# Kernel optimization log

Measured on AMD Instinct MI355X. Metric: run time of the kernel, lower is better.

The kernel has to match this reference:

```python
import jax, jax.numpy as jnp
import numpy as np

EPS = 1e-5

def _ste(x, q):
    # straight-through estimator: forward=q, backward=identity
    return x + jax.lax.stop_gradient(q - x)

def act_quant(x):
    # per-token int8 absmax quantization (BitNet b1.58 style), fake-quantized
    scale = 127.0 / jnp.clip(jnp.max(jnp.abs(x), axis=-1, keepdims=True), EPS)
    q = jnp.clip(jnp.round(x * scale), -128.0, 127.0) / scale
    return _ste(x, q)

def weight_quant(w):
    # ternary {-1,0,1} weights scaled by mean absolute value
    s = jnp.clip(jnp.mean(jnp.abs(w)), EPS)
    q = jnp.clip(jnp.round(w / s), -1.0, 1.0) * s
    return _ste(w, q)

def bit_linear(x, w):
    # x: [..., in], w: [out, in]
    return jnp.einsum('bsi,oi->bso', act_quant(x), weight_quant(w))

def setup_inputs() -> dict:
    key = jax.random.key(0)
    k1, k2, k3 = jax.random.split(key, 3)
    d_model, hidden = 2048, 4 * 2048
    x = jax.random.normal(k1, (4, 2048, d_model), dtype=jnp.float32)
    w1 = jax.random.normal(k2, (hidden, d_model), dtype=jnp.float32) * 0.02
    w2 = jax.random.normal(k3, (d_model, hidden), dtype=jnp.float32) * 0.02
    return {"x": x, "w1": w1, "w2": w2}

def reference(x, w1, w2):
    h = bit_linear(x, w1)            # [B, S, 4*d]
    h = jax.nn.gelu(h, approximate=False)  # exact erf GELU (nn.GELU default)
    return bit_linear(h, w2)         # [B, S, d]
```

## Files before the change

### kernel.cpp

```cpp
#include <hip/hip_runtime.h>
#include <hip/hip_bf16.h>
#include <hip/hip_fp16.h>
#include <stdint.h>

#define TPB 256
#define EPSF 1e-5f

using i32x4 = __attribute__((ext_vector_type(4))) int;


__device__ __forceinline__ void gload16(const void* g, void* l) {
    __builtin_amdgcn_global_load_lds(
        (__attribute__((address_space(1))) void*)g,
        (__attribute__((address_space(3))) void*)l,
        16, 0, 0);
}

__device__ __forceinline__ float wave_reduce_sum(float v) {
#pragma unroll
    for (int off = 32; off > 0; off >>= 1) v += __shfl_down(v, off, 64);
    return v;
}

__device__ __forceinline__ float wave_reduce_max(float v) {
#pragma unroll
    for (int off = 32; off > 0; off >>= 1) v = fmaxf(v, __shfl_down(v, off, 64));
    return v;
}

__device__ __forceinline__ int q8(float f, float scale, float lo, float hi) {
    return (int)fminf(fmaxf(rintf(f * scale), lo), hi);
}

__device__ __forceinline__ float gelu_fast(float x) {
    float x2 = x * x;
    float u = x * (0.7978845608f + 0.0356774081f * x2);
    float e = exp2f(u * -2.8853900817779268f);
    return x * __builtin_amdgcn_rcpf(1.0f + e);
}


__global__ void abssum_partial(const float* __restrict__ w, int n4,
                               float* __restrict__ part) {
    const float4* w4 = (const float4*)w;
    float acc = 0.f;
    for (int i = blockIdx.x * TPB + threadIdx.x; i < n4; i += gridDim.x * TPB) {
        float4 v = w4[i];
        acc += fabsf(v.x) + fabsf(v.y) + fabsf(v.z) + fabsf(v.w);
    }
    acc = wave_reduce_sum(acc);
    __shared__ float sh[4];
    if ((threadIdx.x & 63) == 0) sh[threadIdx.x >> 6] = acc;
    __syncthreads();
    if (threadIdx.x == 0) part[blockIdx.x] = sh[0] + sh[1] + sh[2] + sh[3];
}

__global__ void finalize_scales(const float* __restrict__ part1,
                                const float* __restrict__ part2,
                                float* __restrict__ scales, int nparts, float inv_n) {
    float a = 0.f, b = 0.f;
    for (int i = threadIdx.x; i < nparts; i += TPB) { a += part1[i]; b += part2[i]; }
    a = wave_reduce_sum(a);
    b = wave_reduce_sum(b);
    __shared__ float sa[4], sb[4];
    if ((threadIdx.x & 63) == 0) { sa[threadIdx.x >> 6] = a; sb[threadIdx.x >> 6] = b; }
    __syncthreads();
    if (threadIdx.x == 0) {
        scales[0] = fmaxf((sa[0] + sa[1] + sa[2] + sa[3]) * inv_n, EPSF);
        scales[1] = fmaxf((sb[0] + sb[1] + sb[2] + sb[3]) * inv_n, EPSF);
    }
}


__global__ void quant_w_i8(const float* __restrict__ w,
                           signed char* __restrict__ wq,
                           const float* __restrict__ scales, int sidx, int n4) {
    const float inv = 1.0f / scales[sidx];
    const float4* w4 = (const float4*)w;
    unsigned* oq = (unsigned*)wq;
    for (int i = blockIdx.x * TPB + threadIdx.x; i < n4; i += gridDim.x * TPB) {
        float4 v = w4[i];
        unsigned p = ((unsigned)(q8(v.x, inv, -1.f, 1.f) & 0xff)) |
                     ((unsigned)(q8(v.y, inv, -1.f, 1.f) & 0xff) << 8) |
                     ((unsigned)(q8(v.z, inv, -1.f, 1.f) & 0xff) << 16) |
                     ((unsigned)(q8(v.w, inv, -1.f, 1.f) & 0xff) << 24);
        oq[i] = p;
    }
}


template <int NF4>
__global__ void quant_x_i8(const float* __restrict__ in,
                           signed char* __restrict__ outq,
                           float* __restrict__ dq, int cols) {
    const long long row = blockIdx.x;
    const float4* r4 = (const float4*)(in + row * (long long)cols);
    float4 v[NF4];
    float mx = 0.f;
#pragma unroll
    for (int j = 0; j < NF4; ++j) {
        v[j] = r4[threadIdx.x + TPB * j];
        mx = fmaxf(mx, fmaxf(fmaxf(fabsf(v[j].x), fabsf(v[j].y)),
                             fmaxf(fabsf(v[j].z), fabsf(v[j].w))));
    }
    mx = wave_reduce_max(mx);
    __shared__ float sh[4];
    __shared__ float res;
    if ((threadIdx.x & 63) == 0) sh[threadIdx.x >> 6] = mx;
    __syncthreads();
    if (threadIdx.x == 0) res = fmaxf(fmaxf(sh[0], sh[1]), fmaxf(sh[2], sh[3]));
    __syncthreads();
    const float clipped = fmaxf(res, EPSF);
    const float scale = 127.f / clipped;
    if (threadIdx.x == 0) dq[row] = clipped / 127.f;
    unsigned* oq = (unsigned*)(outq + row * (long long)cols);
#pragma unroll
    for (int j = 0; j < NF4; ++j) {
        unsigned p = ((unsigned)(q8(v[j].x, scale, -128.f, 127.f) & 0xff)) |
                     ((unsigned)(q8(v[j].y, scale, -128.f, 127.f) & 0xff) << 8) |
                     ((unsigned)(q8(v[j].z, scale, -128.f, 127.f) & 0xff) << 16) |
                     ((unsigned)(q8(v[j].w, scale, -128.f, 127.f) & 0xff) << 24);
        oq[threadIdx.x + TPB * j] = p;
    }
}


template <int NJ>
__global__ void quant_h_i8(const unsigned short* __restrict__ h,
                           signed char* __restrict__ outq,
                           float* __restrict__ dq, int cols) {
    const long long row = blockIdx.x;
    const unsigned short* rp = h + row * (long long)cols;
    uint4 v[NJ];
    float mx = 0.f;
#pragma unroll
    for (int j = 0; j < NJ; ++j) {
        v[j] = *(const uint4*)(rp + (threadIdx.x + TPB * j) * 8);
        const unsigned* u = (const unsigned*)&v[j];
#pragma unroll
        for (int e = 0; e < 4; ++e) {
            float2 f2 = __half22float2(*(const __half2*)&u[e]);
            mx = fmaxf(mx, fmaxf(fabsf(f2.x), fabsf(f2.y)));
        }
    }
    mx = wave_reduce_max(mx);
    __shared__ float sh[4];
    __shared__ float res;
    if ((threadIdx.x & 63) == 0) sh[threadIdx.x >> 6] = mx;
    __syncthreads();
    if (threadIdx.x == 0) res = fmaxf(fmaxf(sh[0], sh[1]), fmaxf(sh[2], sh[3]));
    __syncthreads();
    const float clipped = fmaxf(res, EPSF);
    const float scale = 127.f / clipped;
    if (threadIdx.x == 0) dq[row] = clipped / 127.f;
    uint2* oq = (uint2*)(outq + row * (long long)cols);
#pragma unroll
    for (int j = 0; j < NJ; ++j) {
        const unsigned* u = (const unsigned*)&v[j];
        unsigned o[2] = {0, 0};
#pragma unroll
        for (int e = 0; e < 4; ++e) {
            float2 f2 = __half22float2(*(const __half2*)&u[e]);
            unsigned b0 = (unsigned)(q8(f2.x, scale, -128.f, 127.f) & 0xff);
            unsigned b1 = (unsigned)(q8(f2.y, scale, -128.f, 127.f) & 0xff);
            o[e >> 1] |= (b0 | (b1 << 8)) << ((e & 1) * 16);
        }
        oq[threadIdx.x + TPB * j] = *(uint2*)o;
    }
}


__device__ __forceinline__ void stage_half(const char* Xb, long long rowB, int prow,
                                           int tk, char* dst, int tid, int cbs) {
    const long long gc = (long long)tk * 128 + cbs;
    const int r = tid >> 3;
    gload16(Xb + (long long)(prow + r) * rowB + gc, dst + tid * 16);
    gload16(Xb + (long long)(prow + 64 + r) * rowB + gc, dst + 8192 + tid * 16);
}

#define QUAD(MB, NB)                                                            \
    _Pragma("unroll") for (int mi = 0; mi < 4; ++mi)                            \
    _Pragma("unroll") for (int ni = 0; ni < 2; ++ni)                            \
    _Pragma("unroll") for (int ks = 0; ks < 2; ++ks)                            \
        acc[(MB)*4 + mi][(NB)*2 + ni] = __builtin_amdgcn_mfma_i32_16x16x64_i8(  \
            aq[mi][ks], bq[(NB)*2 + ni][ks], acc[(MB)*4 + mi][(NB)*2 + ni], 0, 0, 0);


__global__ __launch_bounds__(512, 2) void gemm1p(
    const signed char* __restrict__ A, const signed char* __restrict__ B,
    unsigned short* __restrict__ C, int N, int K,
    const float* __restrict__ dq, const float* __restrict__ scales, int ntile) {
    __shared__ __align__(16) char lds[131072];

    const int tid = threadIdx.x;
    const int lane = tid & 63;
    const int wid = tid >> 6;
    const int wr = wid >> 2;
    const int wc = wid & 3;

    const unsigned gx = gridDim.x;
    unsigned lin = blockIdx.y * gx + blockIdx.x;
    const unsigned qq = (gx * gridDim.y) >> 3;
    lin = (lin & 7) * qq + (lin >> 3);
    const unsigned bx = lin % gx;
    const unsigned byg = lin / gx;

    const int n0 = (int)bx * 256;
    const long long rb = (long long)K;
    const char* Ab = (const char*)A;
    const char* Bb = (const char*)B;

    const int NTT = ntile << 4;

    const int cbs = (((tid & 7) ^ ((tid >> 3) & 7)) << 4);
    const int l15 = lane & 15, l4 = lane >> 4;
    const int swz = (lane & 7) << 4;
    const int acb0 = (l4 * 16) ^ swz;
    const int acb1 = (64 + l4 * 16) ^ swz;
    const int aoff = wr * 16384;
    const int boff = 32768 + (wc >> 1) * 16384 + (wc & 1) * 8192;

    i32x4 acc[8][4] = {};
    i32x4 aq[4][2], bq[4][2];

    auto mrow = [&](int v) -> int { return ((int)byg * ntile + (v >> 4)) * 256; };

    stage_half(Bb, rb, n0, 0, lds + 32768, tid, cbs);
    stage_half(Bb, rb, n0 + 128, 0, lds + 32768 + 16384, tid, cbs);
    stage_half(Ab, rb, mrow(0), 0, lds + 0, tid, cbs);
    stage_half(Ab, rb, mrow(0) + 128, 0, lds + 16384, tid, cbs);
    stage_half(Bb, rb, n0, 1, lds + 65536 + 32768, tid, cbs);
    stage_half(Bb, rb, n0 + 128, 1, lds + 65536 + 32768 + 16384, tid, cbs);
    stage_half(Ab, rb, mrow(1), 1, lds + 65536, tid, cbs);
    asm volatile("s_waitcnt vmcnt(6)" ::: "memory");
    __builtin_amdgcn_sched_barrier(0);
    __builtin_amdgcn_s_barrier();

    const float s = scales[0];

    for (int vt = 0; vt < NTT; ++vt) {
        char* cur = lds + ((vt & 1) << 16);
        char* nxt = lds + (((vt + 1) & 1) << 16);
        const bool s1 = (vt + 1) < NTT;
        const bool s2 = (vt + 2) < NTT;
        const int k1 = (vt + 1) & 15;
        const int k2 = (vt + 2) & 15;

#pragma unroll
        for (int mi = 0; mi < 4; ++mi) {
            const char* p = cur + aoff + (mi * 16 + l15) * 128;
            aq[mi][0] = *(const i32x4*)(p + acb0);
            aq[mi][1] = *(const i32x4*)(p + acb1);
        }
#pragma unroll
        for (int ni = 0; ni < 4; ++ni) {
            const char* p = cur + boff + (ni * 16 + l15) * 128;
            bq[ni][0] = *(const i32x4*)(p + acb0);
            bq[ni][1] = *(const i32x4*)(p + acb1);
        }
        if (s1) stage_half(Ab, rb, mrow(vt + 1) + 128, k1, nxt + 16384, tid, cbs);
        __builtin_amdgcn_s_setprio(1);
        QUAD(0, 0);
        __builtin_amdgcn_s_setprio(0);
        __builtin_amdgcn_s_barrier();

        if (s2) stage_half(Bb, rb, n0, k2, cur + 32768, tid, cbs);
        __builtin_amdgcn_s_setprio(1);
        QUAD(0, 1);
        __builtin_amdgcn_s_setprio(0);
        __builtin_amdgcn_s_barrier();

#pragma unroll
        for (int mi = 0; mi < 4; ++mi) {
            const char* p = cur + aoff + ((mi + 4) * 16 + l15) * 128;
            aq[mi][0] = *(const i32x4*)(p + acb0);
            aq[mi][1] = *(const i32x4*)(p + acb1);
        }
        if (s2) stage_half(Bb, rb, n0 + 128, k2, cur + 32768 + 16384, tid, cbs);
        __builtin_amdgcn_s_setprio(1);
        QUAD(1, 0);
        __builtin_amdgcn_s_setprio(0);
        __builtin_amdgcn_s_barrier();

        if (s2) stage_half(Ab, rb, mrow(vt + 2), k2, cur, tid, cbs);
        __builtin_amdgcn_s_setprio(1);
        QUAD(1, 1);
        __builtin_amdgcn_s_setprio(0);
        if (s2) { asm volatile("s_waitcnt vmcnt(6)" ::: "memory"); }
        else    { asm volatile("s_waitcnt vmcnt(0)" ::: "memory"); }
        __builtin_amdgcn_sched_barrier(0);
        __builtin_amdgcn_s_barrier();

        if ((vt & 15) == 15) {
            const int m0 = mrow(vt);
#pragma unroll
            for (int mi = 0; mi < 8; ++mi) {
#pragma unroll
                for (int r = 0; r < 4; ++r) {
                    const long long m = m0 + wr * 128 + mi * 16 + l4 * 4 + r;
                    const float f = dq[m] * s;
#pragma unroll
                    for (int ni = 0; ni < 4; ++ni) {
                        const long long n = n0 + wc * 64 + ni * 16 + l15;
                        float v = gelu_fast((float)acc[mi][ni][r] * f);
                        __half hh = __float2half(v);
                        C[m * (long long)N + n] = *(const unsigned short*)&hh;
                        acc[mi][ni][r] = 0;
                    }
                }
            }
        }
    }
}


__global__ __launch_bounds__(512, 2) void gemm2k(
    const signed char* __restrict__ A, const signed char* __restrict__ B,
    float* __restrict__ C, int N, int K,
    const float* __restrict__ dq, const float* __restrict__ scales) {
    __shared__ __align__(16) char lds[131072];

    const int tid = threadIdx.x;
    const int lane = tid & 63;
    const int wid = tid >> 6;
    const int wr = wid >> 2;
    const int wc = wid & 3;

    const unsigned gx = gridDim.x;
    unsigned lin = blockIdx.y * gx + blockIdx.x;
    const unsigned qq = (gx * gridDim.y) >> 3;
    lin = (lin & 7) * qq + (lin >> 3);
    const unsigned bx = lin % gx;
    const unsigned by = lin / gx;

    const long long M0 = (long long)by * 256;
    const long long N0 = (long long)bx * 256;
    const long long rb = (long long)K;
    const char* Ab = (const char*)A + M0 * rb;
    const char* Bb = (const char*)B + N0 * rb;
    const int nt = K >> 7;

    const int cbs = (((tid & 7) ^ ((tid >> 3) & 7)) << 4);
    const int l15 = lane & 15, l4 = lane >> 4;
    const int swz = (lane & 7) << 4;
    const int acb0 = (l4 * 16) ^ swz;
    const int acb1 = (64 + l4 * 16) ^ swz;
    const int aoff = wr * 16384;
    const int boff = 32768 + (wc >> 1) * 16384 + (wc & 1) * 8192;

    i32x4 acc[8][4] = {};
    i32x4 aq[4][2], bq[4][2];

    stage_half(Bb, rb, 0,   0, lds + 32768,         tid, cbs);
    stage_half(Bb, rb, 128, 0, lds + 32768 + 16384, tid, cbs);
    stage_half(Ab, rb, 0,   0, lds + 0,             tid, cbs);
    stage_half(Ab, rb, 128, 0, lds + 16384,         tid, cbs);
    stage_half(Bb, rb, 0,   1, lds + 65536 + 32768,         tid, cbs);
    stage_half(Bb, rb, 128, 1, lds + 65536 + 32768 + 16384, tid, cbs);
    stage_half(Ab, rb, 0,   1, lds + 65536,                 tid, cbs);
    asm volatile("s_waitcnt vmcnt(6)" ::: "memory");
    __builtin_amdgcn_sched_barrier(0);
    __builtin_amdgcn_s_barrier();

    for (int t = 0; t < nt; ++t) {
        char* cur = lds + ((t & 1) << 16);
        char* nxt = lds + (((t + 1) & 1) << 16);
        const bool s1 = (t + 1) < nt;
        const bool s2 = (t + 2) < nt;

#pragma unroll
        for (int mi = 0; mi < 4; ++mi) {
            const char* p = cur + aoff + (mi * 16 + l15) * 128;
            aq[mi][0] = *(const i32x4*)(p + acb0);
            aq[mi][1] = *(const i32x4*)(p + acb1);
        }
#pragma unroll
        for (int ni = 0; ni < 4; ++ni) {
            const char* p = cur + boff + (ni * 16 + l15) * 128;
            bq[ni][0] = *(const i32x4*)(p + acb0);
            bq[ni][1] = *(const i32x4*)(p + acb1);
        }
        if (s1) stage_half(Ab, rb, 128, t + 1, nxt + 16384, tid, cbs);
        __builtin_amdgcn_s_setprio(1);
        QUAD(0, 0);
        __builtin_amdgcn_s_setprio(0);
        __builtin_amdgcn_s_barrier();

        if (s2) stage_half(Bb, rb, 0, t + 2, cur + 32768, tid, cbs);
        __builtin_amdgcn_s_setprio(1);
        QUAD(0, 1);
        __builtin_amdgcn_s_setprio(0);
        __builtin_amdgcn_s_barrier();

#pragma unroll
        for (int mi = 0; mi < 4; ++mi) {
            const char* p = cur + aoff + ((mi + 4) * 16 + l15) * 128;
            aq[mi][0] = *(const i32x4*)(p + acb0);
            aq[mi][1] = *(const i32x4*)(p + acb1);
        }
        if (s2) stage_half(Bb, rb, 128, t + 2, cur + 32768 + 16384, tid, cbs);
        __builtin_amdgcn_s_setprio(1);
        QUAD(1, 0);
        __builtin_amdgcn_s_setprio(0);
        __builtin_amdgcn_s_barrier();

        if (s2) stage_half(Ab, rb, 0, t + 2, cur, tid, cbs);
        __builtin_amdgcn_s_setprio(1);
        QUAD(1, 1);
        __builtin_amdgcn_s_setprio(0);
        if (s2) { asm volatile("s_waitcnt vmcnt(6)" ::: "memory"); }
        else    { asm volatile("s_waitcnt vmcnt(0)" ::: "memory"); }
        __builtin_amdgcn_sched_barrier(0);
        __builtin_amdgcn_s_barrier();
    }

    const float s = scales[1];
#pragma unroll
    for (int mi = 0; mi < 8; ++mi) {
#pragma unroll
        for (int r = 0; r < 4; ++r) {
            const long long m = M0 + wr * 128 + mi * 16 + l4 * 4 + r;
            const float f = dq[m] * s;
#pragma unroll
            for (int ni = 0; ni < 4; ++ni) {
                const long long n = N0 + wc * 64 + ni * 16 + l15;
                __builtin_nontemporal_store(
                    (float)acc[mi][ni][r] * f, C + m * (long long)N + n);
            }
        }
    }
}


extern "C" void kernel_launch(void* const* d_in, const int* in_sizes, int n_in,
                              void* d_out, int out_size, void* d_ws, size_t ws_size,
                              hipStream_t stream) {
    (void)n_in; (void)out_size;
    const float* x  = (const float*)d_in[0];
    const float* w1 = (const float*)d_in[1];
    const float* w2 = (const float*)d_in[2];
    float* out = (float*)d_out;

    const int D = 2048, H = 8192;
    const long long M = (long long)in_sizes[0] / D;

    char* base = (char*)d_ws;
    size_t off = 0;
    auto alloc = [&](size_t bytes) -> char* {
        char* r = base + off;
        off = (off + bytes + 255) & ~(size_t)255;
        return r;
    };

    const bool fullM = ws_size >= (size_t)236 * 1024 * 1024;
    const long long MC = fullM ? M : M / 2;

    float* part1 = (float*)alloc(2048 * 4);
    float* part2 = (float*)alloc(2048 * 4);
    float* scales = (float*)alloc(256);
    float* dqx = (float*)alloc((size_t)M * 4);
    float* dqh = (float*)alloc((size_t)M * 4);
    signed char* wq = (signed char*)alloc((size_t)H * D);
    signed char* xq = (signed char*)alloc((size_t)M * D);
    signed char* hq = (signed char*)alloc((size_t)M * H);
    unsigned short* hf = (unsigned short*)alloc((size_t)MC * H * 2);

    const int nw4 = H * D / 4;
    abssum_partial<<<2048, TPB, 0, stream>>>(w1, nw4, part1);
    abssum_partial<<<2048, TPB, 0, stream>>>(w2, nw4, part2);
    finalize_scales<<<1, TPB, 0, stream>>>(part1, part2, scales, 2048,
                                           1.0f / (float)(H * D));
    quant_w_i8<<<2048, TPB, 0, stream>>>(w1, wq, scales, 0, nw4);
    quant_x_i8<2><<<(int)M, TPB, 0, stream>>>(x, xq, dqx, D);

    if (fullM) {
        gemm1p<<<dim3(32, 8), 512, 0, stream>>>(xq, wq, hf, H, D, dqx, scales, 4);
        quant_h_i8<4><<<(int)M, TPB, 0, stream>>>(hf, hq, dqh, H);
    } else {
        for (int g = 0; g < 2; ++g) {
            const long long m0 = g * MC;
            gemm1p<<<dim3(32, 8), 512, 0, stream>>>(
                xq + m0 * D, wq, hf, H, D, dqx + m0, scales, 2);
            quant_h_i8<4><<<(int)MC, TPB, 0, stream>>>(hf, hq + m0 * H, dqh + m0, H);
        }
    }

    quant_w_i8<<<2048, TPB, 0, stream>>>(w2, wq, scales, 1, nw4);

    gemm2k<<<dim3(D / 256, (int)(M / 256)), 512, 0, stream>>>(
        hq, wq, out, D, H, dqh, scales);
}
```

Measured before the change: 369.8 us.

## Merge weight abssum launches, split B-fragment LDS reads, retile block swizzle

The two abs-sum reduction kernels for w1 and w2 become one 4096-block launch, and finalize reads a single partial buffer. This removes one launch and lets both reductions share the GPU. In both GEMM main loops, the B-fragment LDS reads are split so the second half loads just before the second quad of MFMAs. That lowers register pressure and spreads LDS traffic across the phases. The gemm1 block index remap also changes from a strided XCD interleave to a 2D grouped mapping (8x4 tiles per group) meant to improve L2 reuse per XCD. The new mapping is hardcoded to the 32x8 grid.

New measurement: 358.1 us. 3.2% less time.

```diff
diff --git a/kernel.cpp b/kernel.cpp
--- a/kernel.cpp
+++ b/kernel.cpp
@@ -40,11 +40,13 @@
 }
 
 
-__global__ void abssum_partial(const float* __restrict__ w, int n4,
-                               float* __restrict__ part) {
-    const float4* w4 = (const float4*)w;
+__global__ void abssum2(const float* __restrict__ w1, const float* __restrict__ w2,
+                        int n4, float* __restrict__ part) {
+    const bool second = blockIdx.x >= 2048;
+    const float4* w4 = (const float4*)(second ? w2 : w1);
+    const int b = blockIdx.x & 2047;
     float acc = 0.f;
-    for (int i = blockIdx.x * TPB + threadIdx.x; i < n4; i += gridDim.x * TPB) {
+    for (int i = b * TPB + threadIdx.x; i < n4; i += 2048 * TPB) {
         float4 v = w4[i];
         acc += fabsf(v.x) + fabsf(v.y) + fabsf(v.z) + fabsf(v.w);
     }
@@ -55,11 +57,10 @@
     if (threadIdx.x == 0) part[blockIdx.x] = sh[0] + sh[1] + sh[2] + sh[3];
 }
 
-__global__ void finalize_scales(const float* __restrict__ part1,
-                                const float* __restrict__ part2,
-                                float* __restrict__ scales, int nparts, float inv_n) {
+__global__ void finalize_scales(const float* __restrict__ part,
+                                float* __restrict__ scales, float inv_n) {
     float a = 0.f, b = 0.f;
-    for (int i = threadIdx.x; i < nparts; i += TPB) { a += part1[i]; b += part2[i]; }
+    for (int i = threadIdx.x; i < 2048; i += TPB) { a += part[i]; b += part[i + 2048]; }
     a = wave_reduce_sum(a);
     b = wave_reduce_sum(b);
     __shared__ float sa[4], sb[4];
@@ -185,6 +186,19 @@
         acc[(MB)*4 + mi][(NB)*2 + ni] = __builtin_amdgcn_mfma_i32_16x16x64_i8(  \
             aq[mi][ks], bq[(NB)*2 + ni][ks], acc[(MB)*4 + mi][(NB)*2 + ni], 0, 0, 0);
 
+#define READ_A(base_mi)                                                         \
+    _Pragma("unroll") for (int mi = 0; mi < 4; ++mi) {                          \
+        const char* p = cur + aoff + ((mi + (base_mi)) * 16 + l15) * 128;       \
+        aq[mi][0] = *(const i32x4*)(p + acb0);                                  \
+        aq[mi][1] = *(const i32x4*)(p + acb1);                                  \
+    }
+#define READ_B(n0i, n1i)                                                        \
+    _Pragma("unroll") for (int ni = (n0i); ni < (n1i); ++ni) {                  \
+        const char* p = cur + boff + (ni * 16 + l15) * 128;                     \
+        bq[ni][0] = *(const i32x4*)(p + acb0);                                  \
+        bq[ni][1] = *(const i32x4*)(p + acb1);                                  \
+    }
+
 
 __global__ __launch_bounds__(512, 2) void gemm1p(
     const signed char* __restrict__ A, const signed char* __restrict__ B,
@@ -198,12 +212,10 @@
     const int wr = wid >> 2;
     const int wc = wid & 3;
 
-    const unsigned gx = gridDim.x;
-    unsigned lin = blockIdx.y * gx + blockIdx.x;
-    const unsigned qq = (gx * gridDim.y) >> 3;
-    lin = (lin & 7) * qq + (lin >> 3);
-    const unsigned bx = lin % gx;
-    const unsigned byg = lin / gx;
+    const unsigned orig = blockIdx.y * gridDim.x + blockIdx.x;
+    const unsigned xk = orig & 7, j = orig >> 3;
+    const unsigned bx = (xk & 3) * 8 + (j & 7);
+    const unsigned byg = (xk >> 2) * 4 + (j >> 3);
 
     const int n0 = (int)bx * 256;
     const long long rb = (long long)K;
@@ -246,36 +258,22 @@
         const int k1 = (vt + 1) & 15;
         const int k2 = (vt + 2) & 15;
 
-#pragma unroll
-        for (int mi = 0; mi < 4; ++mi) {
-            const char* p = cur + aoff + (mi * 16 + l15) * 128;
-            aq[mi][0] = *(const i32x4*)(p + acb0);
-            aq[mi][1] = *(const i32x4*)(p + acb1);
-        }
-#pragma unroll
-        for (int ni = 0; ni < 4; ++ni) {
-            const char* p = cur + boff + (ni * 16 + l15) * 128;
-            bq[ni][0] = *(const i32x4*)(p + acb0);
-            bq[ni][1] = *(const i32x4*)(p + acb1);
-        }
+        READ_A(0);
+        READ_B(0, 2);
         if (s1) stage_half(Ab, rb, mrow(vt + 1) + 128, k1, nxt + 16384, tid, cbs);
         __builtin_amdgcn_s_setprio(1);
         QUAD(0, 0);
         __builtin_amdgcn_s_setprio(0);
         __builtin_amdgcn_s_barrier();
 
+        READ_B(2, 4);
         if (s2) stage_half(Bb, rb, n0, k2, cur + 32768, tid, cbs);
         __builtin_amdgcn_s_setprio(1);
         QUAD(0, 1);
         __builtin_amdgcn_s_setprio(0);
         __builtin_amdgcn_s_barrier();
 
-#pragma unroll
-        for (int mi = 0; mi < 4; ++mi) {
-            const char* p = cur + aoff + ((mi + 4) * 16 + l15) * 128;
-            aq[mi][0] = *(const i32x4*)(p + acb0);
-            aq[mi][1] = *(const i32x4*)(p + acb1);
-        }
+        READ_A(4);
         if (s2) stage_half(Bb, rb, n0 + 128, k2, cur + 32768 + 16384, tid, cbs);
         __builtin_amdgcn_s_setprio(1);
         QUAD(1, 0);
@@ -368,36 +366,22 @@
         const bool s1 = (t + 1) < nt;
         const bool s2 = (t + 2) < nt;
 
-#pragma unroll
-        for (int mi = 0; mi < 4; ++mi) {
-            const char* p = cur + aoff + (mi * 16 + l15) * 128;
-            aq[mi][0] = *(const i32x4*)(p + acb0);
-            aq[mi][1] = *(const i32x4*)(p + acb1);
-        }
-#pragma unroll
-        for (int ni = 0; ni < 4; ++ni) {
-            const char* p = cur + boff + (ni * 16 + l15) * 128;
-            bq[ni][0] = *(const i32x4*)(p + acb0);
-            bq[ni][1] = *(const i32x4*)(p + acb1);
-        }
+        READ_A(0);
+        READ_B(0, 2);
         if (s1) stage_half(Ab, rb, 128, t + 1, nxt + 16384, tid, cbs);
         __builtin_amdgcn_s_setprio(1);
         QUAD(0, 0);
         __builtin_amdgcn_s_setprio(0);
         __builtin_amdgcn_s_barrier();
 
+        READ_B(2, 4);
         if (s2) stage_half(Bb, rb, 0, t + 2, cur + 32768, tid, cbs);
         __builtin_amdgcn_s_setprio(1);
         QUAD(0, 1);
         __builtin_amdgcn_s_setprio(0);
         __builtin_amdgcn_s_barrier();
 
-#pragma unroll
-        for (int mi = 0; mi < 4; ++mi) {
-            const char* p = cur + aoff + ((mi + 4) * 16 + l15) * 128;
-            aq[mi][0] = *(const i32x4*)(p + acb0);
-            aq[mi][1] = *(const i32x4*)(p + acb1);
-        }
+        READ_A(4);
         if (s2) stage_half(Bb, rb, 128, t + 2, cur + 32768 + 16384, tid, cbs);
         __builtin_amdgcn_s_setprio(1);
         QUAD(1, 0);
@@ -455,8 +439,7 @@
     const bool fullM = ws_size >= (size_t)236 * 1024 * 1024;
     const long long MC = fullM ? M : M / 2;
 
-    float* part1 = (float*)alloc(2048 * 4);
-    float* part2 = (float*)alloc(2048 * 4);
+    float* part = (float*)alloc(4096 * 4);
     float* scales = (float*)alloc(256);
     float* dqx = (float*)alloc((size_t)M * 4);
     float* dqh = (float*)alloc((size_t)M * 4);
@@ -466,10 +449,8 @@
     unsigned short* hf = (unsigned short*)alloc((size_t)MC * H * 2);
 
     const int nw4 = H * D / 4;
-    abssum_partial<<<2048, TPB, 0, stream>>>(w1, nw4, part1);
-    abssum_partial<<<2048, TPB, 0, stream>>>(w2, nw4, part2);
-    finalize_scales<<<1, TPB, 0, stream>>>(part1, part2, scales, 2048,
-                                           1.0f / (float)(H * D));
+    abssum2<<<4096, TPB, 0, stream>>>(w1, w2, nw4, part);
+    finalize_scales<<<1, TPB, 0, stream>>>(part, scales, 1.0f / (float)(H * D));
     quant_w_i8<<<2048, TPB, 0, stream>>>(w1, wq, scales, 0, nw4);
     quant_x_i8<2><<<(int)M, TPB, 0, stream>>>(x, xq, dqx, D);
 
```
